# Kernel tuning notes

Measured on AMD Instinct MI355X. Metric: run time of the kernel, lower is better.

The kernel has to match this reference:

```python
import jax, jax.numpy as jnp
import numpy as np
import math

FEATURE_DIMS = [32, 64, 96, 128, 192, 256, 384, 512]
HIDDEN = 128
BATCH = 32768


def setup_inputs() -> dict:
    key = jax.random.key(0)
    keys = jax.random.split(key, 2 * len(FEATURE_DIMS) + len(FEATURE_DIMS) + 1)
    inp = {}
    # feature tensors (batch, dim_i)
    for i, d in enumerate(FEATURE_DIMS):
        inp[f"feat{i}"] = jax.random.normal(keys[i], (BATCH, d), dtype=jnp.float32)
    # per-feature key/value projection weights, torch nn.Linear layout (hidden, dim)
    n = len(FEATURE_DIMS)
    for i, d in enumerate(FEATURE_DIMS):
        bound = 1.0 / math.sqrt(d)
        inp[f"Wk{i}"] = jax.random.uniform(keys[n + i], (HIDDEN, d), dtype=jnp.float32, minval=-bound, maxval=bound)
        inp[f"Wv{i}"] = jax.random.uniform(keys[2 * n + i], (HIDDEN, d), dtype=jnp.float32, minval=-bound, maxval=bound)
    inp["query"] = jax.random.normal(keys[-1], (HIDDEN,), dtype=jnp.float32)
    return inp


def reference(feat0, feat1, feat2, feat3, feat4, feat5, feat6, feat7,
              Wk0, Wk1, Wk2, Wk3, Wk4, Wk5, Wk6, Wk7,
              Wv0, Wv1, Wv2, Wv3, Wv4, Wv5, Wv6, Wv7,
              query):
    feats = [feat0, feat1, feat2, feat3, feat4, feat5, feat6, feat7]
    Wks = [Wk0, Wk1, Wk2, Wk3, Wk4, Wk5, Wk6, Wk7]
    Wvs = [Wv0, Wv1, Wv2, Wv3, Wv4, Wv5, Wv6, Wv7]
    # per-feature projections: x @ W.T, torch Linear(bias=False) semantics
    K = jnp.stack([jnp.einsum('bd,hd->bh', f, W) for f, W in zip(feats, Wks)], axis=1)  # (B, F, H)
    V = jnp.stack([jnp.einsum('bd,hd->bh', f, W) for f, W in zip(feats, Wvs)], axis=1)  # (B, F, H)
    scores = jnp.einsum('bfh,h->bf', K, query) / math.sqrt(HIDDEN)  # (B, F)
    attn_weights = jax.nn.softmax(scores, axis=-1)
    combined = jnp.einsum('bf,bfh->bh', attn_weights, V)  # (B, H)
    # dropout is identity in eval mode
    return combined, attn_weights
```

## Files before the change

### kernel.cpp

```cpp
#include <hip/hip_runtime.h>
#include <hip/hip_bf16.h>

#define THREADS 256
#define MTILE   32
#define HID     128
#define BATCH   32768
#define NFEAT   8
#define SDMAX   264

typedef __attribute__((ext_vector_type(4))) float f32x4;
typedef __attribute__((ext_vector_type(8))) short s16x8;

struct Ptrs {
    const float* feat[NFEAT];
    const float* wk[NFEAT];
    const float* wv[NFEAT];
    const float* q;
};

__device__ __forceinline__ float bf2f(unsigned short u) {
    union { unsigned int i; float f; } c; c.i = ((unsigned int)u) << 16; return c.f;
}
__device__ __forceinline__ unsigned short f2bf(float f) {
    union { __hip_bfloat16 h; unsigned short u; } c; c.h = __float2bfloat16(f); return c.u;
}

__device__ const int g_fdim[NFEAT] = {32, 64, 96, 128, 192, 256, 384, 512};
__device__ const int g_foff[NFEAT] = {0, 32, 96, 192, 320, 512, 768, 1152};

__global__ void prep_qk(Ptrs p, float* qk) {
    int i = blockIdx.x;
    int d = g_fdim[i];
    const float* Wk = p.wk[i];
    const float* q  = p.q;
    for (int c = threadIdx.x; c < d; c += blockDim.x) {
        float s = 0.f;
        #pragma unroll 8
        for (int h = 0; h < HID; ++h) s = fmaf(q[h], Wk[h * d + c], s);
        qk[g_foff[i] + c] = s * 0.08838834764831845f;
    }
}

__global__ void prep_wv(Ptrs p, unsigned short* WvB) {
    int fi    = blockIdx.x >> 3;
    int slice = blockIdx.x & 7;
    int D  = g_fdim[fi];
    int Dg = D >> 3;
    const float* Wv = p.wv[fi];
    unsigned short* out = WvB + 128 * g_foff[fi];
    int h0  = slice * 16;
    int cnt = 16 * Dg;
    for (int e = threadIdx.x; e < cnt; e += blockDim.x) {
        int h  = h0 + e / Dg;
        int kg = e - (e / Dg) * Dg;
        const float* src = Wv + h * D + kg * 8;
        float4 x = *reinterpret_cast<const float4*>(src);
        float4 y = *reinterpret_cast<const float4*>(src + 4);
        s16x8 b;
        b[0] = (short)f2bf(x.x); b[1] = (short)f2bf(x.y);
        b[2] = (short)f2bf(x.z); b[3] = (short)f2bf(x.w);
        b[4] = (short)f2bf(y.x); b[5] = (short)f2bf(y.y);
        b[6] = (short)f2bf(y.z); b[7] = (short)f2bf(y.w);
        *reinterpret_cast<s16x8*>(out + (kg * 128 + h) * 8) = b;
    }
}

template<int FI, int D, int CK0, int DC>
__device__ __forceinline__ void stage_issue(const Ptrs& p, int row0, int tid, float4* regs) {
    const float* fbase = p.feat[FI] + (size_t)row0 * D + CK0;
    constexpr int NITER = (MTILE * DC / 4) / THREADS;
    #pragma unroll
    for (int jj = 0; jj < NITER; ++jj) {
        int flat = (tid + jj * THREADS) * 4;
        int r = flat / DC;
        int c = flat - r * DC;
        regs[jj] = *reinterpret_cast<const float4*>(fbase + (size_t)r * D + c);
    }
}

template<int DC>
__device__ __forceinline__ void stage_commit(const float4* regs, unsigned short* A, int tid) {
    constexpr int SD = DC + 8;
    constexpr int NITER = (MTILE * DC / 4) / THREADS;
    #pragma unroll
    for (int jj = 0; jj < NITER; ++jj) {
        int flat = (tid + jj * THREADS) * 4;
        int r = flat / DC;
        int c = flat - r * DC;
        float4 v = regs[jj];
        ushort4 u;
        u.x = f2bf(v.x); u.y = f2bf(v.y); u.z = f2bf(v.z); u.w = f2bf(v.w);
        *reinterpret_cast<ushort4*>(&A[r * SD + c]) = u;
    }
}

template<int FI, int FOFF, int CK0, int DC, bool FIRST, bool LAST>
__device__ __forceinline__ void compute_chunk(
    const unsigned short* A, const unsigned short* WvB, const float* qk,
    float* wAll, float* Zrow, float& spart,
    f32x4 (&P)[2][2], f32x4 (&O)[2][2],
    int tid, int wave, int l15, int q4)
{
    constexpr int SD = DC + 8;
    if (FIRST) {
        spart = 0.f;
        #pragma unroll
        for (int mt = 0; mt < 2; ++mt) {
            P[mt][0] = f32x4{0.f, 0.f, 0.f, 0.f};
            P[mt][1] = f32x4{0.f, 0.f, 0.f, 0.f};
        }
    }

    {
        int r = tid >> 3, part = tid & 7;
        constexpr int Q = DC / 8;
        const float* qf = qk + FOFF + CK0 + part * Q;
        const unsigned short* arow = A + r * SD + part * Q;
        float acc = 0.f;
        #pragma unroll
        for (int c = 0; c < Q; c += 4) {
            ushort4 u  = *reinterpret_cast<const ushort4*>(arow + c);
            float4  qv = *reinterpret_cast<const float4*>(qf + c);
            acc += bf2f(u.x) * qv.x + bf2f(u.y) * qv.y +
                   bf2f(u.z) * qv.z + bf2f(u.w) * qv.w;
        }
        spart += acc;
    }

    {
        const unsigned short* Wb = WvB + 128 * FOFF;
        #pragma unroll
        for (int kk = 0; kk < DC / 32; ++kk) {
            int kg = CK0 / 8 + kk * 4 + q4;
            int hb = wave * 32 + l15;
            s16x8 b0 = *reinterpret_cast<const s16x8*>(Wb + (kg * 128 + hb) * 8);
            s16x8 b1 = *reinterpret_cast<const s16x8*>(Wb + (kg * 128 + hb + 16) * 8);
            int k0 = kk * 32 + q4 * 8;
            #pragma unroll
            for (int mt = 0; mt < 2; ++mt) {
                s16x8 a = *reinterpret_cast<const s16x8*>(A + (mt * 16 + l15) * SD + k0);
                P[mt][0] = __builtin_amdgcn_mfma_f32_16x16x32_bf16(a, b0, P[mt][0], 0, 0, 0);
                P[mt][1] = __builtin_amdgcn_mfma_f32_16x16x32_bf16(a, b1, P[mt][1], 0, 0, 0);
            }
        }
    }

    if (LAST) {
        float s = spart;
        s += __shfl_xor(s, 1, 64);
        s += __shfl_xor(s, 2, 64);
        s += __shfl_xor(s, 4, 64);
        int r = tid >> 3;
        if ((tid & 7) == 0) {
            float w = __expf(s);
            wAll[FI * MTILE + r] = w;
            Zrow[r] += w;
        }
        __syncthreads();
        #pragma unroll
        for (int mt = 0; mt < 2; ++mt) {
            #pragma unroll
            for (int rr = 0; rr < 4; ++rr) {
                float w = wAll[FI * MTILE + mt * 16 + q4 * 4 + rr];
                O[mt][0][rr] += w * P[mt][0][rr];
                O[mt][1][rr] += w * P[mt][1][rr];
            }
        }
    }
}

__global__ __launch_bounds__(THREADS, 4)
void attn_main(Ptrs p, const unsigned short* WvB, const float* qk,
               float* outC, float* outA) {
    __shared__ __align__(16) unsigned short Abuf[2 * MTILE * SDMAX];
    __shared__ float wAll[NFEAT * MTILE];
    __shared__ float Zrow[MTILE];
    unsigned short* buf0 = Abuf;
    unsigned short* buf1 = Abuf + MTILE * SDMAX;

    int tid  = threadIdx.x;
    int wave = tid >> 6;
    int lane = tid & 63;
    int l15  = lane & 15, q4 = lane >> 4;
    int row0 = blockIdx.x * MTILE;

    if (tid < MTILE) Zrow[tid] = 0.f;

    f32x4 P[2][2], O[2][2];
    #pragma unroll
    for (int mt = 0; mt < 2; ++mt) {
        O[mt][0] = f32x4{0.f, 0.f, 0.f, 0.f};
        O[mt][1] = f32x4{0.f, 0.f, 0.f, 0.f};
    }
    float spart = 0.f;
    float4 regs[8];

#define ISSUE(FI,D,CK0,DC)                stage_issue<FI,D,CK0,DC>(p, row0, tid, regs)
#define COMMIT(DC,BUF)                    stage_commit<DC>(regs, BUF, tid)
#define COMP(FI,FOFF,CK0,DC,FIRST,LAST,BUF) \
    compute_chunk<FI,FOFF,CK0,DC,FIRST,LAST>(BUF, WvB, qk, wAll, Zrow, spart, P, O, tid, wave, l15, q4)

    ISSUE(0,  32,   0,  32);                                          COMMIT( 32, buf0); __syncthreads();
    ISSUE(1,  64,   0,  64); COMP(0,    0,   0,  32, true,  true,  buf0); COMMIT( 64, buf1); __syncthreads();
    ISSUE(2,  96,   0,  96); COMP(1,   32,   0,  64, true,  true,  buf1); COMMIT( 96, buf0); __syncthreads();
    ISSUE(3, 128,   0, 128); COMP(2,   96,   0,  96, true,  true,  buf0); COMMIT(128, buf1); __syncthreads();
    ISSUE(4, 192,   0, 192); COMP(3,  192,   0, 128, true,  true,  buf1); COMMIT(192, buf0); __syncthreads();
    ISSUE(5, 256,   0, 256); COMP(4,  320,   0, 192, true,  true,  buf0); COMMIT(256, buf1); __syncthreads();
    ISSUE(6, 384,   0, 256); COMP(5,  512,   0, 256, true,  true,  buf1); COMMIT(256, buf0); __syncthreads();
    ISSUE(6, 384, 256, 128); COMP(6,  768,   0, 256, true,  false, buf0); COMMIT(128, buf1); __syncthreads();
    ISSUE(7, 512,   0, 256); COMP(6,  768, 256, 128, false, true,  buf1); COMMIT(256, buf0); __syncthreads();
    ISSUE(7, 512, 256, 256); COMP(7, 1152,   0, 256, true,  false, buf0); COMMIT(256, buf1); __syncthreads();
                             COMP(7, 1152, 256, 256, false, true,  buf1);

    __syncthreads();
    float* Ctmp = reinterpret_cast<float*>(Abuf);
    #pragma unroll
    for (int mt = 0; mt < 2; ++mt) {
        #pragma unroll
        for (int rr = 0; rr < 4; ++rr) {
            int row = mt * 16 + q4 * 4 + rr;
            float zi = 1.0f / Zrow[row];
            Ctmp[row * 136 + wave * 32 + l15]      = O[mt][0][rr] * zi;
            Ctmp[row * 136 + wave * 32 + 16 + l15] = O[mt][1][rr] * zi;
        }
    }
    __syncthreads();
    #pragma unroll
    for (int it = 0; it < 4; ++it) {
        int j = tid + it * THREADS;
        int r = j >> 5, c4 = (j & 31) * 4;
        *reinterpret_cast<float4*>(outC + (size_t)(row0 + r) * HID + c4) =
            *reinterpret_cast<const float4*>(Ctmp + r * 136 + c4);
    }
    if (tid < MTILE) {
        float zi = 1.0f / Zrow[tid];
        float4 a0, a1;
        a0.x = wAll[0 * MTILE + tid] * zi; a0.y = wAll[1 * MTILE + tid] * zi;
        a0.z = wAll[2 * MTILE + tid] * zi; a0.w = wAll[3 * MTILE + tid] * zi;
        a1.x = wAll[4 * MTILE + tid] * zi; a1.y = wAll[5 * MTILE + tid] * zi;
        a1.z = wAll[6 * MTILE + tid] * zi; a1.w = wAll[7 * MTILE + tid] * zi;
        float* dst = outA + (size_t)(row0 + tid) * NFEAT;
        *reinterpret_cast<float4*>(dst)     = a0;
        *reinterpret_cast<float4*>(dst + 4) = a1;
    }
#undef ISSUE
#undef COMMIT
#undef COMP
}

extern "C" void kernel_launch(void* const* d_in, const int* in_sizes, int n_in,
                              void* d_out, int out_size, void* d_ws, size_t ws_size,
                              hipStream_t stream) {
    Ptrs p;
    for (int i = 0; i < NFEAT; ++i) {
        p.feat[i] = (const float*)d_in[i];
        p.wk[i]   = (const float*)d_in[NFEAT + 2 * i];
        p.wv[i]   = (const float*)d_in[NFEAT + 2 * i + 1];
    }
    p.q = (const float*)d_in[3 * NFEAT];

    unsigned short* WvB = (unsigned short*)d_ws;
    float* qk = (float*)((char*)d_ws + 128 * 1664 * 2);

    prep_wv<<<NFEAT * 8, 256, 0, stream>>>(p, WvB);
    prep_qk<<<NFEAT, 256, 0, stream>>>(p, qk);

    float* outC = (float*)d_out;
    float* outA = outC + (size_t)BATCH * HID;
    attn_main<<<BATCH / MTILE, THREADS, 0, stream>>>(p, WvB, qk, outC, outA);
}
```

Baseline: 348.9 us.

## Deepen feature prefetch pipeline with smaller chunks, LDS-cached qk, fused prep

Restructures the main loop so feature tiles are loaded two chunks ahead using two register sets, capping each chunk at 128 columns to shrink LDS buffers and registers. The qk vector is staged in LDS, barriers become a raw lgkmcnt wait plus s_barrier, and sched_barriers fix the ordering of compute versus issue. The two prep kernels are merged into one launch. The goal is more latency hiding and occupancy, paid for with more barrier stages and a ~6.6KB qk copy per block.

```diff
diff --git a/kernel.cpp b/kernel.cpp
--- a/kernel.cpp
+++ b/kernel.cpp
@@ -6,7 +6,7 @@
 #define HID     128
 #define BATCH   32768
 #define NFEAT   8
-#define SDMAX   264
+#define BUFSZ   (MTILE * 136)
 
 typedef __attribute__((ext_vector_type(4))) float f32x4;
 typedef __attribute__((ext_vector_type(8))) short s16x8;
@@ -27,46 +27,56 @@
 
 __device__ const int g_fdim[NFEAT] = {32, 64, 96, 128, 192, 256, 384, 512};
 __device__ const int g_foff[NFEAT] = {0, 32, 96, 192, 320, 512, 768, 1152};
-
-__global__ void prep_qk(Ptrs p, float* qk) {
-    int i = blockIdx.x;
-    int d = g_fdim[i];
-    const float* Wk = p.wk[i];
-    const float* q  = p.q;
-    for (int c = threadIdx.x; c < d; c += blockDim.x) {
-        float s = 0.f;
-        #pragma unroll 8
-        for (int h = 0; h < HID; ++h) s = fmaf(q[h], Wk[h * d + c], s);
-        qk[g_foff[i] + c] = s * 0.08838834764831845f;
-    }
-}
-
-__global__ void prep_wv(Ptrs p, unsigned short* WvB) {
-    int fi    = blockIdx.x >> 3;
-    int slice = blockIdx.x & 7;
-    int D  = g_fdim[fi];
-    int Dg = D >> 3;
-    const float* Wv = p.wv[fi];
-    unsigned short* out = WvB + 128 * g_foff[fi];
-    int h0  = slice * 16;
-    int cnt = 16 * Dg;
-    for (int e = threadIdx.x; e < cnt; e += blockDim.x) {
-        int h  = h0 + e / Dg;
-        int kg = e - (e / Dg) * Dg;
-        const float* src = Wv + h * D + kg * 8;
-        float4 x = *reinterpret_cast<const float4*>(src);
-        float4 y = *reinterpret_cast<const float4*>(src + 4);
-        s16x8 b;
-        b[0] = (short)f2bf(x.x); b[1] = (short)f2bf(x.y);
-        b[2] = (short)f2bf(x.z); b[3] = (short)f2bf(x.w);
-        b[4] = (short)f2bf(y.x); b[5] = (short)f2bf(y.y);
-        b[6] = (short)f2bf(y.z); b[7] = (short)f2bf(y.w);
-        *reinterpret_cast<s16x8*>(out + (kg * 128 + h) * 8) = b;
-    }
-}
-
-template<int FI, int D, int CK0, int DC>
+constexpr int c_fdim[NFEAT] = {32, 64, 96, 128, 192, 256, 384, 512};
+constexpr int c_foff[NFEAT] = {0, 32, 96, 192, 320, 512, 768, 1152};
+
+__device__ __forceinline__ void sync_lds() {
+    asm volatile("s_waitcnt lgkmcnt(0)" ::: "memory");
+    __builtin_amdgcn_s_barrier();
+    asm volatile("" ::: "memory");
+}
+
+__global__ void prep_all(Ptrs p, unsigned short* WvB, float* qk) {
+    int bid = blockIdx.x;
+    if (bid < NFEAT * 8) {
+        int fi    = bid >> 3;
+        int slice = bid & 7;
+        int D  = g_fdim[fi];
+        int Dg = D >> 3;
+        const float* Wv = p.wv[fi];
+        unsigned short* out = WvB + 128 * g_foff[fi];
+        int h0  = slice * 16;
+        int cnt = 16 * Dg;
+        for (int e = threadIdx.x; e < cnt; e += blockDim.x) {
+            int h  = h0 + e / Dg;
+            int kg = e - (e / Dg) * Dg;
+            const float* src = Wv + h * D + kg * 8;
+            float4 x = *reinterpret_cast<const float4*>(src);
+            float4 y = *reinterpret_cast<const float4*>(src + 4);
+            s16x8 b;
+            b[0] = (short)f2bf(x.x); b[1] = (short)f2bf(x.y);
+            b[2] = (short)f2bf(x.z); b[3] = (short)f2bf(x.w);
+            b[4] = (short)f2bf(y.x); b[5] = (short)f2bf(y.y);
+            b[6] = (short)f2bf(y.z); b[7] = (short)f2bf(y.w);
+            *reinterpret_cast<s16x8*>(out + (kg * 128 + h) * 8) = b;
+        }
+    } else {
+        int i = bid - NFEAT * 8;
+        int d = g_fdim[i];
+        const float* Wk = p.wk[i];
+        const float* q  = p.q;
+        for (int c = threadIdx.x; c < d; c += blockDim.x) {
+            float s = 0.f;
+            #pragma unroll 8
+            for (int h = 0; h < HID; ++h) s = fmaf(q[h], Wk[h * d + c], s);
+            qk[g_foff[i] + c] = s * 0.08838834764831845f;
+        }
+    }
+}
+
+template<int FI, int CK0, int DC>
 __device__ __forceinline__ void stage_issue(const Ptrs& p, int row0, int tid, float4* regs) {
+    constexpr int D = c_fdim[FI];
     const float* fbase = p.feat[FI] + (size_t)row0 * D + CK0;
     constexpr int NITER = (MTILE * DC / 4) / THREADS;
     #pragma unroll
@@ -94,13 +104,14 @@
     }
 }
 
-template<int FI, int FOFF, int CK0, int DC, bool FIRST, bool LAST>
+template<int FI, int CK0, int DC, bool FIRST, bool LAST>
 __device__ __forceinline__ void compute_chunk(
-    const unsigned short* A, const unsigned short* WvB, const float* qk,
+    const unsigned short* A, const unsigned short* WvB, const float* qkS,
     float* wAll, float* Zrow, float& spart,
     f32x4 (&P)[2][2], f32x4 (&O)[2][2],
     int tid, int wave, int l15, int q4)
 {
+    constexpr int FOFF = c_foff[FI];
     constexpr int SD = DC + 8;
     if (FIRST) {
         spart = 0.f;
@@ -114,7 +125,7 @@
     {
         int r = tid >> 3, part = tid & 7;
         constexpr int Q = DC / 8;
-        const float* qf = qk + FOFF + CK0 + part * Q;
+        const float* qf = qkS + FOFF + CK0 + part * Q;
         const unsigned short* arow = A + r * SD + part * Q;
         float acc = 0.f;
         #pragma unroll
@@ -156,7 +167,7 @@
             wAll[FI * MTILE + r] = w;
             Zrow[r] += w;
         }
-        __syncthreads();
+        sync_lds();
         #pragma unroll
         for (int mt = 0; mt < 2; ++mt) {
             #pragma unroll
@@ -172,11 +183,12 @@
 __global__ __launch_bounds__(THREADS, 4)
 void attn_main(Ptrs p, const unsigned short* WvB, const float* qk,
                float* outC, float* outA) {
-    __shared__ __align__(16) unsigned short Abuf[2 * MTILE * SDMAX];
+    __shared__ __align__(16) unsigned short Abuf[2 * BUFSZ];
+    __shared__ __align__(16) float qkS[1664];
     __shared__ float wAll[NFEAT * MTILE];
     __shared__ float Zrow[MTILE];
     unsigned short* buf0 = Abuf;
-    unsigned short* buf1 = Abuf + MTILE * SDMAX;
+    unsigned short* buf1 = Abuf + BUFSZ;
 
     int tid  = threadIdx.x;
     int wave = tid >> 6;
@@ -184,6 +196,7 @@
     int l15  = lane & 15, q4 = lane >> 4;
     int row0 = blockIdx.x * MTILE;
 
+    for (int g = tid; g < 1664; g += THREADS) qkS[g] = qk[g];
     if (tid < MTILE) Zrow[tid] = 0.f;
 
     f32x4 P[2][2], O[2][2];
@@ -193,26 +206,36 @@
         O[mt][1] = f32x4{0.f, 0.f, 0.f, 0.f};
     }
     float spart = 0.f;
-    float4 regs[8];
-
-#define ISSUE(FI,D,CK0,DC)                stage_issue<FI,D,CK0,DC>(p, row0, tid, regs)
-#define COMMIT(DC,BUF)                    stage_commit<DC>(regs, BUF, tid)
-#define COMP(FI,FOFF,CK0,DC,FIRST,LAST,BUF) \
-    compute_chunk<FI,FOFF,CK0,DC,FIRST,LAST>(BUF, WvB, qk, wAll, Zrow, spart, P, O, tid, wave, l15, q4)
-
-    ISSUE(0,  32,   0,  32);                                          COMMIT( 32, buf0); __syncthreads();
-    ISSUE(1,  64,   0,  64); COMP(0,    0,   0,  32, true,  true,  buf0); COMMIT( 64, buf1); __syncthreads();
-    ISSUE(2,  96,   0,  96); COMP(1,   32,   0,  64, true,  true,  buf1); COMMIT( 96, buf0); __syncthreads();
-    ISSUE(3, 128,   0, 128); COMP(2,   96,   0,  96, true,  true,  buf0); COMMIT(128, buf1); __syncthreads();
-    ISSUE(4, 192,   0, 192); COMP(3,  192,   0, 128, true,  true,  buf1); COMMIT(192, buf0); __syncthreads();
-    ISSUE(5, 256,   0, 256); COMP(4,  320,   0, 192, true,  true,  buf0); COMMIT(256, buf1); __syncthreads();
-    ISSUE(6, 384,   0, 256); COMP(5,  512,   0, 256, true,  true,  buf1); COMMIT(256, buf0); __syncthreads();
-    ISSUE(6, 384, 256, 128); COMP(6,  768,   0, 256, true,  false, buf0); COMMIT(128, buf1); __syncthreads();
-    ISSUE(7, 512,   0, 256); COMP(6,  768, 256, 128, false, true,  buf1); COMMIT(256, buf0); __syncthreads();
-    ISSUE(7, 512, 256, 256); COMP(7, 1152,   0, 256, true,  false, buf0); COMMIT(256, buf1); __syncthreads();
-                             COMP(7, 1152, 256, 256, false, true,  buf1);
-
-    __syncthreads();
+    float4 rA[4], rB[4];
+
+#define ISSUE(FI,CK0,DC,R)                stage_issue<FI,CK0,DC>(p, row0, tid, R)
+#define COMMIT(DC,R,BUF)                  stage_commit<DC>(R, BUF, tid)
+#define COMP(FI,CK0,DC,FIRST,LAST,BUF) \
+    compute_chunk<FI,CK0,DC,FIRST,LAST>(BUF, WvB, qkS, wAll, Zrow, spart, P, O, tid, wave, l15, q4)
+#define SB()                              __builtin_amdgcn_sched_barrier(0)
+
+
+    ISSUE(0,   0,  32, rA);  ISSUE(1,   0,  64, rB);
+    COMMIT(32, rA, buf0);
+    sync_lds();
+
+    COMP(0,   0,  32, true,  true,  buf0); SB(); ISSUE(2,   0,  96, rA); SB(); COMMIT( 64, rB, buf1); sync_lds();
+    COMP(1,   0,  64, true,  true,  buf1); SB(); ISSUE(3,   0, 128, rB); SB(); COMMIT( 96, rA, buf0); sync_lds();
+    COMP(2,   0,  96, true,  true,  buf0); SB(); ISSUE(4,   0,  96, rA); SB(); COMMIT(128, rB, buf1); sync_lds();
+    COMP(3,   0, 128, true,  true,  buf1); SB(); ISSUE(4,  96,  96, rB); SB(); COMMIT( 96, rA, buf0); sync_lds();
+    COMP(4,   0,  96, true,  false, buf0); SB(); ISSUE(5,   0, 128, rA); SB(); COMMIT( 96, rB, buf1); sync_lds();
+    COMP(4,  96,  96, false, true,  buf1); SB(); ISSUE(5, 128, 128, rB); SB(); COMMIT(128, rA, buf0); sync_lds();
+    COMP(5,   0, 128, true,  false, buf0); SB(); ISSUE(6,   0, 128, rA); SB(); COMMIT(128, rB, buf1); sync_lds();
+    COMP(5, 128, 128, false, true,  buf1); SB(); ISSUE(6, 128, 128, rB); SB(); COMMIT(128, rA, buf0); sync_lds();
+    COMP(6,   0, 128, true,  false, buf0); SB(); ISSUE(6, 256, 128, rA); SB(); COMMIT(128, rB, buf1); sync_lds();
+    COMP(6, 128, 128, false, false, buf1); SB(); ISSUE(7,   0, 128, rB); SB(); COMMIT(128, rA, buf0); sync_lds();
+    COMP(6, 256, 128, false, true,  buf0); SB(); ISSUE(7, 128, 128, rA); SB(); COMMIT(128, rB, buf1); sync_lds();
+    COMP(7,   0, 128, true,  false, buf1); SB(); ISSUE(7, 256, 128, rB); SB(); COMMIT(128, rA, buf0); sync_lds();
+    COMP(7, 128, 128, false, false, buf0); SB(); ISSUE(7, 384, 128, rA); SB(); COMMIT(128, rB, buf1); sync_lds();
+    COMP(7, 256, 128, false, false, buf1); SB();                               COMMIT(128, rA, buf0); sync_lds();
+    COMP(7, 384, 128, false, true,  buf0);
+
+    sync_lds();
     float* Ctmp = reinterpret_cast<float*>(Abuf);
     #pragma unroll
     for (int mt = 0; mt < 2; ++mt) {
@@ -224,7 +247,7 @@
             Ctmp[row * 136 + wave * 32 + 16 + l15] = O[mt][1][rr] * zi;
         }
     }
-    __syncthreads();
+    sync_lds();
     #pragma unroll
     for (int it = 0; it < 4; ++it) {
         int j = tid + it * THREADS;
@@ -246,6 +269,7 @@
 #undef ISSUE
 #undef COMMIT
 #undef COMP
+#undef SB
 }
 
 extern "C" void kernel_launch(void* const* d_in, const int* in_sizes, int n_in,
@@ -262,8 +286,7 @@
     unsigned short* WvB = (unsigned short*)d_ws;
     float* qk = (float*)((char*)d_ws + 128 * 1664 * 2);
 
-    prep_wv<<<NFEAT * 8, 256, 0, stream>>>(p, WvB);
-    prep_qk<<<NFEAT, 256, 0, stream>>>(p, qk);
+    prep_all<<<NFEAT * 8 + NFEAT, 256, 0, stream>>>(p, WvB, qk);
 
     float* outC = (float*)d_out;
     float* outA = outC + (size_t)BATCH * HID;
```

Measured after the change: 332.0 us. 4.9% less time.

## Load feature tiles directly into MFMA register fragments, dropping LDS staging

Applied to the files above, without the earlier changes.

The main kernel no longer stages bf16 feature tiles through double-buffered LDS with a barrier per chunk. Each lane now loads its own MFMA A-fragment straight from global memory into registers, computes the score dot product from those fp32 values, and prefetches the next 64-wide chunk while the MFMAs run. Softmax weights are broadcast with shuffles instead of LDS, the qk vector is cached in shared memory, and the two prep kernels are merged into one launch. This removes LDS traffic and per-chunk syncs, at the cost of more registers and less coalesced global loads (32-byte row segments per lane).

```diff
diff --git a/kernel.cpp b/kernel.cpp
--- a/kernel.cpp
+++ b/kernel.cpp
@@ -6,7 +6,6 @@
 #define HID     128
 #define BATCH   32768
 #define NFEAT   8
-#define SDMAX   264
 
 typedef __attribute__((ext_vector_type(4))) float f32x4;
 typedef __attribute__((ext_vector_type(8))) short s16x8;
@@ -18,153 +17,147 @@
     const float* q;
 };
 
-__device__ __forceinline__ float bf2f(unsigned short u) {
-    union { unsigned int i; float f; } c; c.i = ((unsigned int)u) << 16; return c.f;
-}
 __device__ __forceinline__ unsigned short f2bf(float f) {
     union { __hip_bfloat16 h; unsigned short u; } c; c.h = __float2bfloat16(f); return c.u;
 }
 
+__device__ __forceinline__ s16x8 pack8(float4 x, float4 y) {
+    s16x8 b;
+    b[0] = (short)f2bf(x.x); b[1] = (short)f2bf(x.y);
+    b[2] = (short)f2bf(x.z); b[3] = (short)f2bf(x.w);
+    b[4] = (short)f2bf(y.x); b[5] = (short)f2bf(y.y);
+    b[6] = (short)f2bf(y.z); b[7] = (short)f2bf(y.w);
+    return b;
+}
+
 __device__ const int g_fdim[NFEAT] = {32, 64, 96, 128, 192, 256, 384, 512};
 __device__ const int g_foff[NFEAT] = {0, 32, 96, 192, 320, 512, 768, 1152};
-
-__global__ void prep_qk(Ptrs p, float* qk) {
-    int i = blockIdx.x;
-    int d = g_fdim[i];
-    const float* Wk = p.wk[i];
-    const float* q  = p.q;
-    for (int c = threadIdx.x; c < d; c += blockDim.x) {
-        float s = 0.f;
-        #pragma unroll 8
-        for (int h = 0; h < HID; ++h) s = fmaf(q[h], Wk[h * d + c], s);
-        qk[g_foff[i] + c] = s * 0.08838834764831845f;
-    }
-}
-
-__global__ void prep_wv(Ptrs p, unsigned short* WvB) {
-    int fi    = blockIdx.x >> 3;
-    int slice = blockIdx.x & 7;
-    int D  = g_fdim[fi];
-    int Dg = D >> 3;
-    const float* Wv = p.wv[fi];
-    unsigned short* out = WvB + 128 * g_foff[fi];
-    int h0  = slice * 16;
-    int cnt = 16 * Dg;
-    for (int e = threadIdx.x; e < cnt; e += blockDim.x) {
-        int h  = h0 + e / Dg;
-        int kg = e - (e / Dg) * Dg;
-        const float* src = Wv + h * D + kg * 8;
-        float4 x = *reinterpret_cast<const float4*>(src);
-        float4 y = *reinterpret_cast<const float4*>(src + 4);
-        s16x8 b;
-        b[0] = (short)f2bf(x.x); b[1] = (short)f2bf(x.y);
-        b[2] = (short)f2bf(x.z); b[3] = (short)f2bf(x.w);
-        b[4] = (short)f2bf(y.x); b[5] = (short)f2bf(y.y);
-        b[6] = (short)f2bf(y.z); b[7] = (short)f2bf(y.w);
-        *reinterpret_cast<s16x8*>(out + (kg * 128 + h) * 8) = b;
-    }
-}
-
-template<int FI, int D, int CK0, int DC>
-__device__ __forceinline__ void stage_issue(const Ptrs& p, int row0, int tid, float4* regs) {
-    const float* fbase = p.feat[FI] + (size_t)row0 * D + CK0;
-    constexpr int NITER = (MTILE * DC / 4) / THREADS;
-    #pragma unroll
-    for (int jj = 0; jj < NITER; ++jj) {
-        int flat = (tid + jj * THREADS) * 4;
-        int r = flat / DC;
-        int c = flat - r * DC;
-        regs[jj] = *reinterpret_cast<const float4*>(fbase + (size_t)r * D + c);
-    }
-}
-
-template<int DC>
-__device__ __forceinline__ void stage_commit(const float4* regs, unsigned short* A, int tid) {
-    constexpr int SD = DC + 8;
-    constexpr int NITER = (MTILE * DC / 4) / THREADS;
-    #pragma unroll
-    for (int jj = 0; jj < NITER; ++jj) {
-        int flat = (tid + jj * THREADS) * 4;
-        int r = flat / DC;
-        int c = flat - r * DC;
-        float4 v = regs[jj];
-        ushort4 u;
-        u.x = f2bf(v.x); u.y = f2bf(v.y); u.z = f2bf(v.z); u.w = f2bf(v.w);
-        *reinterpret_cast<ushort4*>(&A[r * SD + c]) = u;
-    }
-}
-
-template<int FI, int FOFF, int CK0, int DC, bool FIRST, bool LAST>
-__device__ __forceinline__ void compute_chunk(
-    const unsigned short* A, const unsigned short* WvB, const float* qk,
-    float* wAll, float* Zrow, float& spart,
-    f32x4 (&P)[2][2], f32x4 (&O)[2][2],
-    int tid, int wave, int l15, int q4)
-{
-    constexpr int SD = DC + 8;
+constexpr int c_fdim[NFEAT] = {32, 64, 96, 128, 192, 256, 384, 512};
+constexpr int c_foff[NFEAT] = {0, 32, 96, 192, 320, 512, 768, 1152};
+
+__global__ void prep_all(Ptrs p, unsigned short* WvB, float* qk) {
+    int bid = blockIdx.x;
+    if (bid < NFEAT * 8) {
+        int fi    = bid >> 3;
+        int slice = bid & 7;
+        int D  = g_fdim[fi];
+        int Dg = D >> 3;
+        const float* Wv = p.wv[fi];
+        unsigned short* out = WvB + 128 * g_foff[fi];
+        int h0  = slice * 16;
+        int cnt = 16 * Dg;
+        for (int e = threadIdx.x; e < cnt; e += blockDim.x) {
+            int h  = h0 + e / Dg;
+            int kg = e - (e / Dg) * Dg;
+            const float* src = Wv + h * D + kg * 8;
+            float4 x = *reinterpret_cast<const float4*>(src);
+            float4 y = *reinterpret_cast<const float4*>(src + 4);
+            *reinterpret_cast<s16x8*>(out + (kg * 128 + h) * 8) = pack8(x, y);
+        }
+    } else {
+        int i = bid - NFEAT * 8;
+        int d = g_fdim[i];
+        const float* Wk = p.wk[i];
+        const float* q  = p.q;
+        for (int c = threadIdx.x; c < d; c += blockDim.x) {
+            float s = 0.f;
+            #pragma unroll 8
+            for (int h = 0; h < HID; ++h) s = fmaf(q[h], Wk[h * d + c], s);
+            qk[g_foff[i] + c] = s * 0.08838834764831845f;
+        }
+    }
+}
+
+
+template<int FI, int CK0, int DC>
+__device__ __forceinline__ void loadA(const Ptrs& p, int row0, int l15, int q4, float4* fA) {
+    constexpr int D  = c_fdim[FI];
+    constexpr int KK = DC / 32;
+    const float* b = p.feat[FI] + (size_t)(row0 + l15) * D + CK0 + q4 * 8;
+    #pragma unroll
+    for (int mt = 0; mt < 2; ++mt) {
+        const float* bb = b + mt * 16 * D;
+        #pragma unroll
+        for (int kk = 0; kk < KK; ++kk) {
+            fA[(mt * KK + kk) * 2 + 0] = *reinterpret_cast<const float4*>(bb + kk * 32);
+            fA[(mt * KK + kk) * 2 + 1] = *reinterpret_cast<const float4*>(bb + kk * 32 + 4);
+        }
+    }
+}
+
+template<int FI, int CK0, int DC>
+__device__ __forceinline__ void loadB(const unsigned short* WvB, int wave, int l15, int q4,
+                                      s16x8 (&bf)[2][2]) {
+    constexpr int FOFF = c_foff[FI];
+    constexpr int KK = DC / 32;
+    const unsigned short* Wb = WvB + 128 * FOFF;
+    int hb = wave * 32 + l15;
+    #pragma unroll
+    for (int kk = 0; kk < KK; ++kk) {
+        int kg = CK0 / 8 + kk * 4 + q4;
+        bf[kk][0] = *reinterpret_cast<const s16x8*>(Wb + (kg * 128 + hb) * 8);
+        bf[kk][1] = *reinterpret_cast<const s16x8*>(Wb + (kg * 128 + hb + 16) * 8);
+    }
+}
+
+template<int FI, int CK0, int DC, bool FIRST>
+__device__ __forceinline__ void score_cvt(const float4* fA, const float* qkS, int q4,
+                                          float (&spart)[2], s16x8 (&af)[2][2],
+                                          f32x4 (&P)[2][2]) {
+    constexpr int FOFF = c_foff[FI];
+    constexpr int KK = DC / 32;
     if (FIRST) {
-        spart = 0.f;
+        spart[0] = spart[1] = 0.f;
+        P[0][0] = P[0][1] = P[1][0] = P[1][1] = f32x4{0.f, 0.f, 0.f, 0.f};
+    }
+    #pragma unroll
+    for (int kk = 0; kk < KK; ++kk) {
+        float4 q0 = *reinterpret_cast<const float4*>(qkS + FOFF + CK0 + kk * 32 + q4 * 8);
+        float4 q1 = *reinterpret_cast<const float4*>(qkS + FOFF + CK0 + kk * 32 + q4 * 8 + 4);
         #pragma unroll
         for (int mt = 0; mt < 2; ++mt) {
-            P[mt][0] = f32x4{0.f, 0.f, 0.f, 0.f};
-            P[mt][1] = f32x4{0.f, 0.f, 0.f, 0.f};
-        }
-    }
-
-    {
-        int r = tid >> 3, part = tid & 7;
-        constexpr int Q = DC / 8;
-        const float* qf = qk + FOFF + CK0 + part * Q;
-        const unsigned short* arow = A + r * SD + part * Q;
-        float acc = 0.f;
-        #pragma unroll
-        for (int c = 0; c < Q; c += 4) {
-            ushort4 u  = *reinterpret_cast<const ushort4*>(arow + c);
-            float4  qv = *reinterpret_cast<const float4*>(qf + c);
-            acc += bf2f(u.x) * qv.x + bf2f(u.y) * qv.y +
-                   bf2f(u.z) * qv.z + bf2f(u.w) * qv.w;
-        }
-        spart += acc;
-    }
-
-    {
-        const unsigned short* Wb = WvB + 128 * FOFF;
-        #pragma unroll
-        for (int kk = 0; kk < DC / 32; ++kk) {
-            int kg = CK0 / 8 + kk * 4 + q4;
-            int hb = wave * 32 + l15;
-            s16x8 b0 = *reinterpret_cast<const s16x8*>(Wb + (kg * 128 + hb) * 8);
-            s16x8 b1 = *reinterpret_cast<const s16x8*>(Wb + (kg * 128 + hb + 16) * 8);
-            int k0 = kk * 32 + q4 * 8;
-            #pragma unroll
-            for (int mt = 0; mt < 2; ++mt) {
-                s16x8 a = *reinterpret_cast<const s16x8*>(A + (mt * 16 + l15) * SD + k0);
-                P[mt][0] = __builtin_amdgcn_mfma_f32_16x16x32_bf16(a, b0, P[mt][0], 0, 0, 0);
-                P[mt][1] = __builtin_amdgcn_mfma_f32_16x16x32_bf16(a, b1, P[mt][1], 0, 0, 0);
-            }
-        }
-    }
-
+            float4 x = fA[(mt * KK + kk) * 2 + 0];
+            float4 y = fA[(mt * KK + kk) * 2 + 1];
+            spart[mt] += x.x * q0.x + x.y * q0.y + x.z * q0.z + x.w * q0.w
+                       + y.x * q1.x + y.y * q1.y + y.z * q1.z + y.w * q1.w;
+            af[mt][kk] = pack8(x, y);
+        }
+    }
+}
+
+template<int FI, int DC, bool LAST>
+__device__ __forceinline__ void mfma_tail(const s16x8 (&af)[2][2], const s16x8 (&bf)[2][2],
+                                          f32x4 (&P)[2][2], f32x4 (&O)[2][2],
+                                          float (&spart)[2], float (&Zacc)[2],
+                                          float* wAll, int tid, int lane, int l15, int q4) {
+    constexpr int KK = DC / 32;
+    #pragma unroll
+    for (int kk = 0; kk < KK; ++kk) {
+        #pragma unroll
+        for (int mt = 0; mt < 2; ++mt) {
+            P[mt][0] = __builtin_amdgcn_mfma_f32_16x16x32_bf16(af[mt][kk], bf[kk][0], P[mt][0], 0, 0, 0);
+            P[mt][1] = __builtin_amdgcn_mfma_f32_16x16x32_bf16(af[mt][kk], bf[kk][1], P[mt][1], 0, 0, 0);
+        }
+    }
     if (LAST) {
-        float s = spart;
-        s += __shfl_xor(s, 1, 64);
-        s += __shfl_xor(s, 2, 64);
-        s += __shfl_xor(s, 4, 64);
-        int r = tid >> 3;
-        if ((tid & 7) == 0) {
+        int sb = (lane & 48);
+        int wb = sb + q4 * 4;
+        #pragma unroll
+        for (int mt = 0; mt < 2; ++mt) {
+            float s = spart[mt];
+            s += __shfl_xor(s, 16, 64);
+            s += __shfl_xor(s, 32, 64);
             float w = __expf(s);
-            wAll[FI * MTILE + r] = w;
-            Zrow[r] += w;
-        }
-        __syncthreads();
-        #pragma unroll
-        for (int mt = 0; mt < 2; ++mt) {
-            #pragma unroll
-            for (int rr = 0; rr < 4; ++rr) {
-                float w = wAll[FI * MTILE + mt * 16 + q4 * 4 + rr];
-                O[mt][0][rr] += w * P[mt][0][rr];
-                O[mt][1][rr] += w * P[mt][1][rr];
-            }
+            Zacc[mt] += w;
+            if (tid < 16) wAll[FI * MTILE + mt * 16 + l15] = w;
+            float w0 = __shfl(w, wb + 0, 64);
+            float w1 = __shfl(w, wb + 1, 64);
+            float w2 = __shfl(w, wb + 2, 64);
+            float w3 = __shfl(w, wb + 3, 64);
+            O[mt][0][0] += w0 * P[mt][0][0]; O[mt][0][1] += w1 * P[mt][0][1];
+            O[mt][0][2] += w2 * P[mt][0][2]; O[mt][0][3] += w3 * P[mt][0][3];
+            O[mt][1][0] += w0 * P[mt][1][0]; O[mt][1][1] += w1 * P[mt][1][1];
+            O[mt][1][2] += w2 * P[mt][1][2]; O[mt][1][3] += w3 * P[mt][1][3];
         }
     }
 }
@@ -172,54 +165,84 @@
 __global__ __launch_bounds__(THREADS, 4)
 void attn_main(Ptrs p, const unsigned short* WvB, const float* qk,
                float* outC, float* outA) {
-    __shared__ __align__(16) unsigned short Abuf[2 * MTILE * SDMAX];
+    __shared__ __align__(16) float smem[MTILE * 136];
     __shared__ float wAll[NFEAT * MTILE];
-    __shared__ float Zrow[MTILE];
-    unsigned short* buf0 = Abuf;
-    unsigned short* buf1 = Abuf + MTILE * SDMAX;
+    __shared__ float ZAll[MTILE];
 
     int tid  = threadIdx.x;
     int wave = tid >> 6;
     int lane = tid & 63;
     int l15  = lane & 15, q4 = lane >> 4;
     int row0 = blockIdx.x * MTILE;
-
-    if (tid < MTILE) Zrow[tid] = 0.f;
-
-    f32x4 P[2][2], O[2][2];
+    float* qkS = smem;
+
+    float4 fA[8];
+    s16x8  af[2][2], bf[2][2];
+    f32x4  P[2][2], O[2][2];
+    float  spart[2], Zacc[2];
+    Zacc[0] = Zacc[1] = 0.f;
     #pragma unroll
     for (int mt = 0; mt < 2; ++mt) {
         O[mt][0] = f32x4{0.f, 0.f, 0.f, 0.f};
         O[mt][1] = f32x4{0.f, 0.f, 0.f, 0.f};
     }
-    float spart = 0.f;
-    float4 regs[8];
-
-#define ISSUE(FI,D,CK0,DC)                stage_issue<FI,D,CK0,DC>(p, row0, tid, regs)
-#define COMMIT(DC,BUF)                    stage_commit<DC>(regs, BUF, tid)
-#define COMP(FI,FOFF,CK0,DC,FIRST,LAST,BUF) \
-    compute_chunk<FI,FOFF,CK0,DC,FIRST,LAST>(BUF, WvB, qk, wAll, Zrow, spart, P, O, tid, wave, l15, q4)
-
-    ISSUE(0,  32,   0,  32);                                          COMMIT( 32, buf0); __syncthreads();
-    ISSUE(1,  64,   0,  64); COMP(0,    0,   0,  32, true,  true,  buf0); COMMIT( 64, buf1); __syncthreads();
-    ISSUE(2,  96,   0,  96); COMP(1,   32,   0,  64, true,  true,  buf1); COMMIT( 96, buf0); __syncthreads();
-    ISSUE(3, 128,   0, 128); COMP(2,   96,   0,  96, true,  true,  buf0); COMMIT(128, buf1); __syncthreads();
-    ISSUE(4, 192,   0, 192); COMP(3,  192,   0, 128, true,  true,  buf1); COMMIT(192, buf0); __syncthreads();
-    ISSUE(5, 256,   0, 256); COMP(4,  320,   0, 192, true,  true,  buf0); COMMIT(256, buf1); __syncthreads();
-    ISSUE(6, 384,   0, 256); COMP(5,  512,   0, 256, true,  true,  buf1); COMMIT(256, buf0); __syncthreads();
-    ISSUE(6, 384, 256, 128); COMP(6,  768,   0, 256, true,  false, buf0); COMMIT(128, buf1); __syncthreads();
-    ISSUE(7, 512,   0, 256); COMP(6,  768, 256, 128, false, true,  buf1); COMMIT(256, buf0); __syncthreads();
-    ISSUE(7, 512, 256, 256); COMP(7, 1152,   0, 256, true,  false, buf0); COMMIT(256, buf1); __syncthreads();
-                             COMP(7, 1152, 256, 256, false, true,  buf1);
-
+
+    loadA<0, 0, 32>(p, row0, l15, q4, fA);
+    for (int g = tid; g < 1664; g += THREADS) qkS[g] = qk[g];
     __syncthreads();
-    float* Ctmp = reinterpret_cast<float*>(Abuf);
+
+#define STEP(FI, CK0, DC, FIRST, LAST, NFI, NCK0, NDC)                          \
+    loadB<FI, CK0, DC>(WvB, wave, l15, q4, bf);                                 \
+    score_cvt<FI, CK0, DC, FIRST>(fA, qkS, q4, spart, af, P);                   \
+    loadA<NFI, NCK0, NDC>(p, row0, l15, q4, fA);                                \
+    __builtin_amdgcn_sched_barrier(0);                                          \
+    mfma_tail<FI, DC, LAST>(af, bf, P, O, spart, Zacc, wAll, tid, lane, l15, q4);
+
+#define STEPLAST(FI, CK0, DC, FIRST, LAST)                                      \
+    loadB<FI, CK0, DC>(WvB, wave, l15, q4, bf);                                 \
+    score_cvt<FI, CK0, DC, FIRST>(fA, qkS, q4, spart, af, P);                   \
+    mfma_tail<FI, DC, LAST>(af, bf, P, O, spart, Zacc, wAll, tid, lane, l15, q4);
+
+    STEP(0,   0, 32, true,  true,   1,   0, 64)
+    STEP(1,   0, 64, true,  true,   2,   0, 64)
+    STEP(2,   0, 64, true,  false,  2,  64, 32)
+    STEP(2,  64, 32, false, true,   3,   0, 64)
+    STEP(3,   0, 64, true,  false,  3,  64, 64)
+    STEP(3,  64, 64, false, true,   4,   0, 64)
+    STEP(4,   0, 64, true,  false,  4,  64, 64)
+    STEP(4,  64, 64, false, false,  4, 128, 64)
+    STEP(4, 128, 64, false, true,   5,   0, 64)
+    STEP(5,   0, 64, true,  false,  5,  64, 64)
+    STEP(5,  64, 64, false, false,  5, 128, 64)
+    STEP(5, 128, 64, false, false,  5, 192, 64)
+    STEP(5, 192, 64, false, true,   6,   0, 64)
+    STEP(6,   0, 64, true,  false,  6,  64, 64)
+    STEP(6,  64, 64, false, false,  6, 128, 64)
+    STEP(6, 128, 64, false, false,  6, 192, 64)
+    STEP(6, 192, 64, false, false,  6, 256, 64)
+    STEP(6, 256, 64, false, false,  6, 320, 64)
+    STEP(6, 320, 64, false, true,   7,   0, 64)
+    STEP(7,   0, 64, true,  false,  7,  64, 64)
+    STEP(7,  64, 64, false, false,  7, 128, 64)
+    STEP(7, 128, 64, false, false,  7, 192, 64)
+    STEP(7, 192, 64, false, false,  7, 256, 64)
+    STEP(7, 256, 64, false, false,  7, 320, 64)
+    STEP(7, 320, 64, false, false,  7, 384, 64)
+    STEP(7, 384, 64, false, false,  7, 448, 64)
+    STEPLAST(7, 448, 64, false, true)
+#undef STEP
+#undef STEPLAST
+
+    if (tid < 16) { ZAll[tid] = Zacc[0]; ZAll[16 + tid] = Zacc[1]; }
+    __syncthreads();
+
+    float* Ctmp = smem;
     #pragma unroll
     for (int mt = 0; mt < 2; ++mt) {
         #pragma unroll
         for (int rr = 0; rr < 4; ++rr) {
             int row = mt * 16 + q4 * 4 + rr;
-            float zi = 1.0f / Zrow[row];
+            float zi = 1.0f / ZAll[row];
             Ctmp[row * 136 + wave * 32 + l15]      = O[mt][0][rr] * zi;
             Ctmp[row * 136 + wave * 32 + 16 + l15] = O[mt][1][rr] * zi;
         }
@@ -233,7 +256,7 @@
             *reinterpret_cast<const float4*>(Ctmp + r * 136 + c4);
     }
     if (tid < MTILE) {
-        float zi = 1.0f / Zrow[tid];
+        float zi = 1.0f / ZAll[tid];
         float4 a0, a1;
         a0.x = wAll[0 * MTILE + tid] * zi; a0.y = wAll[1 * MTILE + tid] * zi;
         a0.z = wAll[2 * MTILE + tid] * zi; a0.w = wAll[3 * MTILE + tid] * zi;
@@ -243,9 +266,6 @@
         *reinterpret_cast<float4*>(dst)     = a0;
         *reinterpret_cast<float4*>(dst + 4) = a1;
     }
-#undef ISSUE
-#undef COMMIT
-#undef COMP
 }
 
 extern "C" void kernel_launch(void* const* d_in, const int* in_sizes, int n_in,
@@ -262,8 +282,7 @@
     unsigned short* WvB = (unsigned short*)d_ws;
     float* qk = (float*)((char*)d_ws + 128 * 1664 * 2);
 
-    prep_wv<<<NFEAT * 8, 256, 0, stream>>>(p, WvB);
-    prep_qk<<<NFEAT, 256, 0, stream>>>(p, qk);
+    prep_all<<<NFEAT * 8 + NFEAT, 256, 0, stream>>>(p, WvB, qk);
 
     float* outC = (float*)d_out;
     float* outA = outC + (size_t)BATCH * HID;
```

New measurement: 863.7 us. +147.5%, slower.
